# Optimization experiments

Hardware: AMD Instinct MI355X
Metric: run time of the kernel (lower is better)

The kernel has to match this reference:

```python
import jax, jax.numpy as jnp
import numpy as np

B, S, M, D, H = 2, 2048, 512, 1024, 16
HD = D // H      # head dim 64
KVC = D // 16    # MLA kv compression dim 64
QC = D // 32     # MLA q compression dim 32
RD = HD          # retrieval (qk) head dim 64
LOOKBACK = 8     # cross_window
EPS = 1e-6


def rmsnorm(x, w):
    return x * jax.lax.rsqrt(jnp.mean(x * x, axis=-1, keepdims=True) + EPS) * w


def setup_inputs():
    key = jax.random.key(0)
    ks = jax.random.split(key, 20)
    g = lambda i, shape: jax.random.normal(ks[i], shape, jnp.float32) * 0.02
    return {
        "x": jax.random.normal(ks[0], (B, S, D), jnp.float32),
        "memory": jax.random.normal(ks[1], (B, M, D), jnp.float32),
        "seg_ids": jnp.sort(jax.random.randint(ks[2], (B, S), 0, M), axis=-1),
        "norm1_w": jnp.ones((D,), jnp.float32),
        "W_dq": g(3, (D, QC)),
        "W_uq": g(4, (QC, H * RD)),
        "W_dkv": g(5, (D, KVC)),
        "W_uk": g(6, (KVC, H * RD)),
        "W_uv": g(7, (KVC, H * HD)),
        "W_o_self": g(8, (H * HD, D)),
        "norm2_w": jnp.ones((D,), jnp.float32),
        "W_q_c": g(9, (D, D)),
        "W_k_c": g(10, (D, D)),
        "W_v_c": g(11, (D, D)),
        "W_o_c": g(12, (D, D)),
        "norm3_w": jnp.ones((D,), jnp.float32),
        "W_gate": g(13, (D, 4 * D)),
        "W_up": g(14, (D, 4 * D)),
        "W_down": g(15, (4 * D, D)),
    }


def reference(x, memory, seg_ids, norm1_w, W_dq, W_uq, W_dkv, W_uk, W_uv,
              W_o_self, norm2_w, W_q_c, W_k_c, W_v_c, W_o_c, norm3_w,
              W_gate, W_up, W_down):
    # ---- MLA causal self-attention (low-rank compressed q/kv) ----
    h = rmsnorm(x, norm1_w)
    q = ((h @ W_dq) @ W_uq).reshape(B, S, H, RD)
    c_kv = h @ W_dkv                                  # [B,S,KVC]
    k = (c_kv @ W_uk).reshape(B, S, H, RD)
    v = (c_kv @ W_uv).reshape(B, S, H, HD)
    scores = jnp.einsum('bihd,bjhd->bhij', q, k) / np.float32(np.sqrt(RD))
    causal = jnp.tril(jnp.ones((S, S), bool))
    scores = jnp.where(causal, scores, -jnp.inf)
    attn = jax.nn.softmax(scores, axis=-1)
    o = jnp.einsum('bhij,bjhd->bihd', attn, v).reshape(B, S, H * HD)
    x = x + o @ W_o_self
    # ---- segment sliding-window cross-attention ----
    h = rmsnorm(x, norm2_w)
    qc = (h @ W_q_c).reshape(B, S, H, HD)
    kc = (memory @ W_k_c).reshape(B, M, H, HD)
    vc = (memory @ W_v_c).reshape(B, M, H, HD)
    sc = jnp.einsum('bihd,bjhd->bhij', qc, kc) / np.float32(np.sqrt(HD))
    kv_pos = jnp.arange(M)
    seg = seg_ids[:, :, None]                          # [B,S,1]
    allowed = (kv_pos[None, None, :] <= seg) & (kv_pos[None, None, :] >= seg - LOOKBACK)
    sc = jnp.where(allowed[:, None, :, :], sc, -jnp.inf)
    ac = jax.nn.softmax(sc, axis=-1)
    oc = jnp.einsum('bhij,bjhd->bihd', ac, vc).reshape(B, S, D)
    x = x + oc @ W_o_c
    # ---- SwiGLU FFN ----
    h = rmsnorm(x, norm3_w)
    x = x + (jax.nn.silu(h @ W_gate) * (h @ W_up)) @ W_down
    return x
```

## Files before the change

### kernel.cpp

```cpp
#include <hip/hip_runtime.h>
#include <stdint.h>

typedef unsigned short U16;
typedef __bf16 bf16x8 __attribute__((ext_vector_type(8)));
typedef unsigned short us8 __attribute__((ext_vector_type(8)));
typedef float f32x4 __attribute__((ext_vector_type(4)));

__device__ __forceinline__ U16 f2bf(float f) {
    unsigned u = __builtin_bit_cast(unsigned, f);
    unsigned r = (u + 0x7fff + ((u >> 16) & 1)) >> 16;
    return (U16)r;
}
__device__ __forceinline__ U16 f2bf_fast(float f) {
    return (U16)((__builtin_bit_cast(unsigned, f) + 0x8000u) >> 16);
}
__device__ __forceinline__ float bf2f(U16 v) {
    return __builtin_bit_cast(float, (unsigned)v << 16);
}
__device__ __forceinline__ bf16x8 ld8(const U16* p) { return __builtin_bit_cast(bf16x8, *(const us8*)p); }

__device__ __forceinline__ void async16(const U16* g, U16* l) {
    auto* gp = (const __attribute__((address_space(1))) U16*)g;
    auto* lp = (__attribute__((address_space(3))) U16*)(uintptr_t)(uint32_t)(uintptr_t)l;
    __builtin_amdgcn_global_load_lds(gp, lp, 16, 0, 0);
}

struct WEnt { const float* src; U16* dst; int K, N, Kpad, Npad, koff, noff, tiles; };
struct WTable { WEnt e[13]; };

__global__ __launch_bounds__(256) void wtrans_all(WTable t) {
    int bx = blockIdx.x, ei = 0;
    while (bx >= t.e[ei].tiles) { bx -= t.e[ei].tiles; ei++; }
    const WEnt E = t.e[ei];
    const int ntn = E.Npad >> 5;
    const int n0 = (bx % ntn) * 32, k0 = (bx / ntn) * 32;
    __shared__ float tile[32][33];
    const int tx = threadIdx.x & 31, ty = threadIdx.x >> 5;
#pragma unroll
    for (int i = 0; i < 4; i++) {
        int kk = k0 + ty + i * 8, n = n0 + tx;
        int k = kk - E.koff;
        float v = (k >= 0 && k < E.K && n < E.N) ? E.src[(size_t)k * E.N + n] : 0.f;
        tile[ty + i * 8][tx] = v;
    }
    __syncthreads();
#pragma unroll
    for (int i = 0; i < 4; i++) {
        int n = n0 + ty + i * 8, kk = k0 + tx;
        E.dst[(size_t)(E.noff + n) * E.Kpad + kk] = f2bf(tile[tx][ty + i * 8]);
    }
}

__global__ __launch_bounds__(256) void f2bf_k(const float* __restrict__ in, U16* __restrict__ out, int n) {
    int i = (blockIdx.x * 256 + threadIdx.x) * 4;
    if (i < n) {
        float4 v = *(const float4*)(in + i);
        out[i + 0] = f2bf(v.x); out[i + 1] = f2bf(v.y);
        out[i + 2] = f2bf(v.z); out[i + 3] = f2bf(v.w);
    }
}

__global__ __launch_bounds__(256) void cq_reduce(const float* __restrict__ p, U16* __restrict__ out) {
    int i = (blockIdx.x * 256 + threadIdx.x) * 4;
    const float4 a = *(const float4*)(p + i);
    const float4 b = *(const float4*)(p + 524288 + i);
    const float4 c = *(const float4*)(p + 2 * 524288 + i);
    const float4 d = *(const float4*)(p + 3 * 524288 + i);
    out[i + 0] = f2bf(a.x + b.x + c.x + d.x);
    out[i + 1] = f2bf(a.y + b.y + c.y + d.y);
    out[i + 2] = f2bf(a.z + b.z + c.z + d.z);
    out[i + 3] = f2bf(a.w + b.w + c.w + d.w);
}

__global__ __launch_bounds__(256) void rmsnorm_k(const float* __restrict__ x, const float* __restrict__ w,
                                                 U16* __restrict__ h) {
    const int row = blockIdx.x, tid = threadIdx.x;
    const float4 v = *(const float4*)(x + (size_t)row * 1024 + tid * 4);
    float ss = v.x * v.x + v.y * v.y + v.z * v.z + v.w * v.w;
#pragma unroll
    for (int o = 32; o > 0; o >>= 1) ss += __shfl_xor(ss, o);
    __shared__ float red[4];
    if ((tid & 63) == 0) red[tid >> 6] = ss;
    __syncthreads();
    float tot = red[0] + red[1] + red[2] + red[3];
    float sc = rsqrtf(tot * (1.0f / 1024.0f) + 1e-6f);
    const float4 wv = *(const float4*)(w + tid * 4);
    U16* hp = h + (size_t)row * 1024 + tid * 4;
    hp[0] = f2bf(v.x * sc * wv.x); hp[1] = f2bf(v.y * sc * wv.y);
    hp[2] = f2bf(v.z * sc * wv.z); hp[3] = f2bf(v.w * sc * wv.w);
}

__global__ __launch_bounds__(256) void qkuv_gemm(const U16* __restrict__ A, const U16* __restrict__ Wuqk,
                                                 const U16* __restrict__ Wuv,
                                                 U16* __restrict__ qkb, U16* __restrict__ vt) {
    __shared__ __align__(16) U16 As[2][128 * 32];
    __shared__ __align__(16) U16 Bs[2][128 * 32];
    __shared__ __align__(16) U16 Ts[4][64 * 80];
    const int tid = threadIdx.x;
    const bool isuv = blockIdx.x >= 16;
    const U16* Bt = isuv ? Wuv : Wuqk;
    const int n0 = (isuv ? blockIdx.x - 16 : blockIdx.x) * 128;
    const int m0 = blockIdx.y * 128;
    const int wave = tid >> 6, lane = tid & 63, l16 = lane & 15, quad = lane >> 4;
    const int wm = (wave >> 1) * 64, wn = (wave & 1) * 64;
    const int sr = lane >> 2, sc = (lane & 3) * 8;
    const U16* gA = A + (size_t)(m0 + wave * 32 + sr) * 128 + sc;
    const U16* gB = Bt + (size_t)(n0 + wave * 32 + sr) * 128 + sc;
    f32x4 acc[4][4] = {};
    for (int kt = 0; kt < 128; kt += 64) {
        __syncthreads();
#pragma unroll
        for (int p = 0; p < 2; p++) {
            const int o = kt + p * 32;
            async16(gA + o, &As[p][(wave * 32) * 32]);
            async16(gA + 16 * 128 + o, &As[p][(wave * 32 + 16) * 32]);
            async16(gB + o, &Bs[p][(wave * 32) * 32]);
            async16(gB + 16 * 128 + o, &Bs[p][(wave * 32 + 16) * 32]);
        }
        __syncthreads();
#pragma unroll
        for (int p = 0; p < 2; p++) {
            bf16x8 af[4], bfr[4];
#pragma unroll
            for (int i = 0; i < 4; i++) {
                af[i]  = ld8(&As[p][(wm + i * 16 + l16) * 32 + quad * 8]);
                bfr[i] = ld8(&Bs[p][(wn + i * 16 + l16) * 32 + quad * 8]);
            }
#pragma unroll
            for (int mi = 0; mi < 4; mi++)
#pragma unroll
                for (int ni = 0; ni < 4; ni++)
                    acc[mi][ni] = __builtin_amdgcn_mfma_f32_16x16x32_bf16(af[mi], bfr[ni], acc[mi][ni], 0, 0, 0);
        }
    }
    if (isuv) {
        U16* T = Ts[wave];
#pragma unroll
        for (int mi = 0; mi < 4; mi++)
#pragma unroll
            for (int ni = 0; ni < 4; ni++)
#pragma unroll
                for (int r = 0; r < 4; r++)
                    T[(ni * 16 + l16) * 80 + mi * 16 + quad * 4 + r] = f2bf(acc[mi][ni][r]);
#pragma unroll
        for (int c = 0; c < 8; c++) {
            int nloc = (lane >> 3) + 8 * c, mloc = (lane & 7) * 8;
            us8 v = *(const us8*)&T[nloc * 80 + mloc];
            *(us8*)&vt[(size_t)(n0 + wn + nloc) * 4096 + (m0 + wm + mloc)] = v;
        }
    } else {
#pragma unroll
        for (int mi = 0; mi < 4; mi++)
#pragma unroll
            for (int r = 0; r < 4; r++) {
                int m = m0 + wm + mi * 16 + quad * 4 + r;
#pragma unroll
                for (int ni = 0; ni < 4; ni++)
                    qkb[(size_t)m * 2048 + n0 + wn + ni * 16 + l16] = f2bf(acc[mi][ni][r]);
            }
    }
}

template <int EPI>
__global__ __launch_bounds__(256) void gemm_m64(const U16* __restrict__ A, const U16* __restrict__ Bt,
                                                void* __restrict__ Cout, const float* __restrict__ resid,
                                                int M, int N, int K, int lda, int ldb, int ldc) {
    __shared__ __align__(16) U16 As[4][64 * 32];
    __shared__ __align__(16) U16 Bs[4][128 * 32];
    const int tid = threadIdx.x;
    const int m0 = blockIdx.y * 64, n0 = blockIdx.x * 128;
    const int k0 = blockIdx.z * K;
    const int wave = tid >> 6, lane = tid & 63, l16 = lane & 15, quad = lane >> 4;
    const int wm = (wave >> 1) * 32, wn = (wave & 1) * 64;
    const int sr = lane >> 2, sc = (lane & 3) * 8;
    const U16* gA = A + (size_t)(m0 + wave * 16 + sr) * lda + sc + k0;
    const U16* gB = Bt + (size_t)(n0 + wave * 32 + sr) * ldb + sc + k0;
    f32x4 acc[2][4] = {};
    for (int kt = 0; kt < K; kt += 128) {
        __syncthreads();
#pragma unroll
        for (int p = 0; p < 4; p++) {
            const int o = kt + p * 32;
            async16(gA + o, &As[p][(wave * 16) * 32]);
            async16(gB + o, &Bs[p][(wave * 32) * 32]);
            async16(gB + (size_t)16 * ldb + o, &Bs[p][(wave * 32 + 16) * 32]);
        }
        __syncthreads();
#pragma unroll
        for (int p = 0; p < 4; p++) {
            bf16x8 af[2], bfr[4];
#pragma unroll
            for (int i = 0; i < 2; i++)
                af[i] = ld8(&As[p][(wm + i * 16 + l16) * 32 + quad * 8]);
#pragma unroll
            for (int i = 0; i < 4; i++)
                bfr[i] = ld8(&Bs[p][(wn + i * 16 + l16) * 32 + quad * 8]);
#pragma unroll
            for (int mi = 0; mi < 2; mi++)
#pragma unroll
                for (int ni = 0; ni < 4; ni++)
                    acc[mi][ni] = __builtin_amdgcn_mfma_f32_16x16x32_bf16(af[mi], bfr[ni], acc[mi][ni], 0, 0, 0);
        }
    }
#pragma unroll
    for (int mi = 0; mi < 2; mi++) {
#pragma unroll
        for (int r = 0; r < 4; r++) {
            int m = m0 + wm + mi * 16 + quad * 4 + r;
#pragma unroll
            for (int ni = 0; ni < 4; ni++) {
                int n = n0 + wn + ni * 16 + l16;
                float val = acc[mi][ni][r];
                if (EPI == 0) ((U16*)Cout)[(size_t)m * ldc + n] = f2bf(val);
                else if (EPI == 1) ((float*)Cout)[(size_t)m * ldc + n] = resid[(size_t)m * ldc + n] + val;
                else if (EPI == 5) ((float*)Cout)[(size_t)blockIdx.z * 524288 + (size_t)m * ldc + n] = val;
            }
        }
    }
}

__global__ __launch_bounds__(256) void qckv_gemm(const U16* __restrict__ hbuf, const U16* __restrict__ Wqc,
                                                 const U16* __restrict__ memb, const U16* __restrict__ Wkvc,
                                                 U16* __restrict__ qcb, U16* __restrict__ kvcb) {
    __shared__ __align__(16) U16 As[4][64 * 32];
    __shared__ __align__(16) U16 Bs[4][128 * 32];
    const int tid = threadIdx.x, bid = blockIdx.x;
    const U16 *A, *Bt; U16* C; int m0, n0, ldc;
    if (bid < 512) { A = hbuf; Bt = Wqc;  C = qcb;  m0 = (bid >> 3) * 64; n0 = (bid & 7) * 128;  ldc = 1024; }
    else { int b2 = bid - 512; A = memb; Bt = Wkvc; C = kvcb; m0 = (b2 >> 4) * 64; n0 = (b2 & 15) * 128; ldc = 2048; }
    const int wave = tid >> 6, lane = tid & 63, l16 = lane & 15, quad = lane >> 4;
    const int wm = (wave >> 1) * 32, wn = (wave & 1) * 64;
    const int sr = lane >> 2, sc = (lane & 3) * 8;
    const U16* gA = A + (size_t)(m0 + wave * 16 + sr) * 1024 + sc;
    const U16* gB = Bt + (size_t)(n0 + wave * 32 + sr) * 1024 + sc;
    f32x4 acc[2][4] = {};
    for (int kt = 0; kt < 1024; kt += 128) {
        __syncthreads();
#pragma unroll
        for (int p = 0; p < 4; p++) {
            const int o = kt + p * 32;
            async16(gA + o, &As[p][(wave * 16) * 32]);
            async16(gB + o, &Bs[p][(wave * 32) * 32]);
            async16(gB + 16 * 1024 + o, &Bs[p][(wave * 32 + 16) * 32]);
        }
        __syncthreads();
#pragma unroll
        for (int p = 0; p < 4; p++) {
            bf16x8 af[2], bfr[4];
#pragma unroll
            for (int i = 0; i < 2; i++)
                af[i] = ld8(&As[p][(wm + i * 16 + l16) * 32 + quad * 8]);
#pragma unroll
            for (int i = 0; i < 4; i++)
                bfr[i] = ld8(&Bs[p][(wn + i * 16 + l16) * 32 + quad * 8]);
#pragma unroll
            for (int mi = 0; mi < 2; mi++)
#pragma unroll
                for (int ni = 0; ni < 4; ni++)
                    acc[mi][ni] = __builtin_amdgcn_mfma_f32_16x16x32_bf16(af[mi], bfr[ni], acc[mi][ni], 0, 0, 0);
        }
    }
#pragma unroll
    for (int mi = 0; mi < 2; mi++)
#pragma unroll
        for (int r = 0; r < 4; r++) {
            int m = m0 + wm + mi * 16 + quad * 4 + r;
#pragma unroll
            for (int ni = 0; ni < 4; ni++)
                C[(size_t)m * ldc + n0 + wn + ni * 16 + l16] = f2bf(acc[mi][ni][r]);
        }
}

__global__ __launch_bounds__(256) void ffn1_fused(const U16* __restrict__ A, const U16* __restrict__ Wgu,
                                                  U16* __restrict__ Cout) {
    __shared__ __align__(16) U16 As[2][128 * 32];
    __shared__ __align__(16) U16 Gs[2][64 * 32];
    __shared__ __align__(16) U16 Us[2][64 * 32];
    const int tid = threadIdx.x;
    const int m0 = blockIdx.y * 128, n0 = blockIdx.x * 64;
    const int wave = tid >> 6, lane = tid & 63, l16 = lane & 15, quad = lane >> 4;
    const int wm = (wave >> 1) * 64, wn = (wave & 1) * 32;
    const int sr = lane >> 2, sc = (lane & 3) * 8;
    const U16* gA = A + (size_t)(m0 + wave * 32 + sr) * 1024 + sc;
    const U16* gG = Wgu + (size_t)(n0 + wave * 16 + sr) * 1024 + sc;
    const U16* gU = gG + (size_t)4096 * 1024;
    f32x4 ag[4][2] = {}, au[4][2] = {};
    for (int kt = 0; kt < 1024; kt += 64) {
        __syncthreads();
#pragma unroll
        for (int p = 0; p < 2; p++) {
            const int o = kt + p * 32;
            async16(gA + o, &As[p][(wave * 32) * 32]);
            async16(gA + 16 * 1024 + o, &As[p][(wave * 32 + 16) * 32]);
            async16(gG + o, &Gs[p][(wave * 16) * 32]);
            async16(gU + o, &Us[p][(wave * 16) * 32]);
        }
        __syncthreads();
#pragma unroll
        for (int p = 0; p < 2; p++) {
            bf16x8 af[4], bg[2], bu[2];
#pragma unroll
            for (int i = 0; i < 4; i++)
                af[i] = ld8(&As[p][(wm + i * 16 + l16) * 32 + quad * 8]);
#pragma unroll
            for (int i = 0; i < 2; i++) {
                bg[i] = ld8(&Gs[p][(wn + i * 16 + l16) * 32 + quad * 8]);
                bu[i] = ld8(&Us[p][(wn + i * 16 + l16) * 32 + quad * 8]);
            }
#pragma unroll
            for (int mi = 0; mi < 4; mi++)
#pragma unroll
                for (int ni = 0; ni < 2; ni++) {
                    ag[mi][ni] = __builtin_amdgcn_mfma_f32_16x16x32_bf16(af[mi], bg[ni], ag[mi][ni], 0, 0, 0);
                    au[mi][ni] = __builtin_amdgcn_mfma_f32_16x16x32_bf16(af[mi], bu[ni], au[mi][ni], 0, 0, 0);
                }
        }
    }
#pragma unroll
    for (int mi = 0; mi < 4; mi++) {
#pragma unroll
        for (int r = 0; r < 4; r++) {
            int m = m0 + wm + mi * 16 + quad * 4 + r;
#pragma unroll
            for (int ni = 0; ni < 2; ni++) {
                int n = n0 + wn + ni * 16 + l16;
                float g = ag[mi][ni][r], u = au[mi][ni][r];
                float act = g / (1.f + __expf(-g)) * u;
                Cout[(size_t)m * 4096 + n] = f2bf(act);
            }
        }
    }
}

__global__ __launch_bounds__(256) void flash_self3(const U16* __restrict__ QK, const U16* __restrict__ Vt,
                                                   U16* __restrict__ Og) {
    __shared__ __align__(16) U16 Ps[4 * 1280];
    __shared__ float Ored[4 * 2080];
    __shared__ float Lred[128];
    const int wave = threadIdx.x >> 6, lane = threadIdx.x & 63;
    const int l16 = lane & 15, quad = lane >> 4;
    const int bx = blockIdx.x;
    const int t = 63 - (bx >> 5);
    const int bh = bx & 31, b = bh >> 4, h = bh & 15;
    const int q0 = t * 32;
    const size_t rowQ0 = (size_t)(b * 2048 + q0 + l16) * 2048 + h * 64;
    const size_t rowQ1 = rowQ0 + 16 * 2048;
    bf16x8 aq[2][2];
    aq[0][0] = ld8(QK + rowQ0 + quad * 8);  aq[0][1] = ld8(QK + rowQ0 + 32 + quad * 8);
    aq[1][0] = ld8(QK + rowQ1 + quad * 8);  aq[1][1] = ld8(QK + rowQ1 + 32 + quad * 8);
    const U16* Kbase = QK + (size_t)(b * 2048) * 2048 + 1024 + h * 64;
    const U16* Vbase = Vt + (size_t)(h * 64) * 4096 + b * 2048;
    f32x4 o[2][4] = {};
    float ls[2][4] = {};
    U16* Pw = &Ps[wave * 1280];
    const int prd = l16 * 40 + ((quad ^ (l16 >> 2)) << 3);
    const int jend = q0 + 32;
    for (int j0 = wave * 32; j0 < jend; j0 += 128) {
        const U16* kp = Kbase + (size_t)j0 * 2048;
        bf16x8 b00 = ld8(kp + (size_t)l16 * 2048 + quad * 8);
        bf16x8 b01 = ld8(kp + (size_t)l16 * 2048 + 32 + quad * 8);
        bf16x8 b10 = ld8(kp + (size_t)(16 + l16) * 2048 + quad * 8);
        bf16x8 b11 = ld8(kp + (size_t)(16 + l16) * 2048 + 32 + quad * 8);
        bf16x8 v0 = ld8(Vbase + (size_t)(0  + l16) * 4096 + j0 + quad * 8);
        bf16x8 v1 = ld8(Vbase + (size_t)(16 + l16) * 4096 + j0 + quad * 8);
        bf16x8 v2 = ld8(Vbase + (size_t)(32 + l16) * 4096 + j0 + quad * 8);
        bf16x8 v3 = ld8(Vbase + (size_t)(48 + l16) * 4096 + j0 + quad * 8);
        f32x4 s[2][2] = {};
#pragma unroll
        for (int g = 0; g < 2; g++) {
            s[g][0] = __builtin_amdgcn_mfma_f32_16x16x32_bf16(aq[g][0], b00, s[g][0], 0, 0, 0);
            s[g][0] = __builtin_amdgcn_mfma_f32_16x16x32_bf16(aq[g][1], b01, s[g][0], 0, 0, 0);
            s[g][1] = __builtin_amdgcn_mfma_f32_16x16x32_bf16(aq[g][0], b10, s[g][1], 0, 0, 0);
            s[g][1] = __builtin_amdgcn_mfma_f32_16x16x32_bf16(aq[g][1], b11, s[g][1], 0, 0, 0);
        }
        float p0[2][4], p1[2][4];
        if (j0 + 32 >= jend) {
#pragma unroll
            for (int g = 0; g < 2; g++)
#pragma unroll
                for (int r = 0; r < 4; r++) {
                    int qg = q0 + g * 16 + quad * 4 + r;
                    p0[g][r] = (j0 + l16 <= qg) ? __expf(fminf(s[g][0][r] * 0.125f, 30.f)) : 0.f;
                    p1[g][r] = (j0 + 16 + l16 <= qg) ? __expf(fminf(s[g][1][r] * 0.125f, 30.f)) : 0.f;
                }
        } else {
#pragma unroll
            for (int g = 0; g < 2; g++)
#pragma unroll
                for (int r = 0; r < 4; r++) {
                    p0[g][r] = __expf(fminf(s[g][0][r] * 0.125f, 30.f));
                    p1[g][r] = __expf(fminf(s[g][1][r] * 0.125f, 30.f));
                }
        }
#pragma unroll
        for (int g = 0; g < 2; g++)
#pragma unroll
            for (int r = 0; r < 4; r++) {
                ls[g][r] += p0[g][r] + p1[g][r];
                int row = quad * 4 + r;
                Pw[g * 640 + row * 40 + ((((l16 >> 3) + 0) ^ quad) << 3) + (l16 & 7)] = f2bf_fast(p0[g][r]);
                Pw[g * 640 + row * 40 + ((((l16 >> 3) + 2) ^ quad) << 3) + (l16 & 7)] = f2bf_fast(p1[g][r]);
            }
#pragma unroll
        for (int g = 0; g < 2; g++) {
            bf16x8 ap = ld8(&Pw[g * 640 + prd]);
            o[g][0] = __builtin_amdgcn_mfma_f32_16x16x32_bf16(ap, v0, o[g][0], 0, 0, 0);
            o[g][1] = __builtin_amdgcn_mfma_f32_16x16x32_bf16(ap, v1, o[g][1], 0, 0, 0);
            o[g][2] = __builtin_amdgcn_mfma_f32_16x16x32_bf16(ap, v2, o[g][2], 0, 0, 0);
            o[g][3] = __builtin_amdgcn_mfma_f32_16x16x32_bf16(ap, v3, o[g][3], 0, 0, 0);
        }
    }
    float* Or = &Ored[wave * 2080];
#pragma unroll
    for (int g = 0; g < 2; g++) {
#pragma unroll
        for (int dg = 0; dg < 4; dg++)
#pragma unroll
            for (int r = 0; r < 4; r++)
                Or[(g * 16 + quad * 4 + r) * 65 + dg * 16 + l16] = o[g][dg][r];
#pragma unroll
        for (int r = 0; r < 4; r++) {
            float v = ls[g][r];
            v += __shfl_xor(v, 1); v += __shfl_xor(v, 2);
            v += __shfl_xor(v, 4); v += __shfl_xor(v, 8);
            if (l16 == 0) Lred[wave * 32 + g * 16 + quad * 4 + r] = v;
        }
    }
    __syncthreads();
    const int q = threadIdx.x >> 3, d0 = (threadIdx.x & 7) * 8;
    float l = Lred[q] + Lred[32 + q] + Lred[64 + q] + Lred[96 + q];
    float inv = 1.0f / l;
    us8 outv;
#pragma unroll
    for (int i = 0; i < 8; i++) {
        int idx = q * 65 + d0 + i;
        float s = Ored[idx] + Ored[2080 + idx] + Ored[4160 + idx] + Ored[6240 + idx];
        outv[i] = f2bf(s * inv);
    }
    *(us8*)(Og + (size_t)(b * 2048 + q0 + q) * 1024 + h * 64 + d0) = outv;
}

__global__ __launch_bounds__(256) void cross_attn(const U16* __restrict__ qc, const U16* __restrict__ kvc,
                                                  const int* __restrict__ seg_ids, U16* __restrict__ oc) {
    const int tok = blockIdx.x;
    const int b = tok >> 11;
    const int w = threadIdx.x >> 6, lane = threadIdx.x & 63;
    const int h = blockIdx.y * 4 + w;
    const int seg = seg_ids[tok];
    const size_t qoff = (size_t)tok * 1024 + h * 64 + lane;
    float q = bf2f(qc[qoff]);
    float s[9];
#pragma unroll
    for (int jj = 0; jj < 9; jj++) {
        int j = seg - 8 + jj;
        float sc = -INFINITY;
        if (j >= 0) {
            float kv = bf2f(kvc[((size_t)(b * 512) + j) * 2048 + h * 64 + lane]);
            sc = q * kv;
            sc += __shfl_xor(sc, 1); sc += __shfl_xor(sc, 2); sc += __shfl_xor(sc, 4);
            sc += __shfl_xor(sc, 8); sc += __shfl_xor(sc, 16); sc += __shfl_xor(sc, 32);
            sc *= 0.125f;
        }
        s[jj] = sc;
    }
    float m = s[0];
#pragma unroll
    for (int jj = 1; jj < 9; jj++) m = fmaxf(m, s[jj]);
    float l = 0.f, o = 0.f;
#pragma unroll
    for (int jj = 0; jj < 9; jj++) {
        int j = seg - 8 + jj;
        if (j >= 0) {
            float p = __expf(s[jj] - m);
            l += p;
            o += p * bf2f(kvc[((size_t)(b * 512) + j) * 2048 + 1024 + h * 64 + lane]);
        }
    }
    oc[qoff] = f2bf(o / l);
}

extern "C" void kernel_launch(void* const* d_in, const int* in_sizes, int n_in,
                              void* d_out, int out_size, void* d_ws, size_t ws_size,
                              hipStream_t stream) {
    const float* x      = (const float*)d_in[0];
    const float* memory = (const float*)d_in[1];
    const int*   seg    = (const int*)d_in[2];
    const float* n1w    = (const float*)d_in[3];
    const float* W_dq   = (const float*)d_in[4];
    const float* W_uq   = (const float*)d_in[5];
    const float* W_dkv  = (const float*)d_in[6];
    const float* W_uk   = (const float*)d_in[7];
    const float* W_uv   = (const float*)d_in[8];
    const float* W_os   = (const float*)d_in[9];
    const float* n2w    = (const float*)d_in[10];
    const float* W_qc   = (const float*)d_in[11];
    const float* W_kc   = (const float*)d_in[12];
    const float* W_vc   = (const float*)d_in[13];
    const float* W_oc   = (const float*)d_in[14];
    const float* n3w    = (const float*)d_in[15];
    const float* W_gate = (const float*)d_in[16];
    const float* W_up   = (const float*)d_in[17];
    const float* W_down = (const float*)d_in[18];
    (void)in_sizes; (void)n_in; (void)out_size; (void)ws_size;

    char* ws = (char*)d_ws;
    size_t off = 0;
    auto alloc = [&](size_t bytes) -> void* {
        void* p = ws + off;
        off += (bytes + 255) & ~(size_t)255;
        return p;
    };
    const size_t MB = 1024 * 1024;
    U16* hbuf     = (U16*)alloc(8 * MB);
    float* x1     = (float*)alloc(16 * MB);
    float* x2     = (float*)alloc(16 * MB);
    float* cq32   = (float*)alloc(8 * MB);
    U16* Wt_dqkv  = (U16*)alloc(128 * 1024 * 2);
    U16* Wt_uqk   = (U16*)alloc(2048 * 128 * 2);
    U16* Wt_uv    = (U16*)alloc(1024 * 128 * 2);
    U16* Wt_os    = (U16*)alloc(1024 * 1024 * 2);
    U16* Wt_qc    = (U16*)alloc(1024 * 1024 * 2);
    U16* Wt_kvc   = (U16*)alloc((size_t)2048 * 1024 * 2);
    U16* Wt_oc    = (U16*)alloc(1024 * 1024 * 2);
    U16* Wt_gu    = (U16*)alloc((size_t)8192 * 1024 * 2);
    U16* Wt_down  = (U16*)alloc((size_t)1024 * 4096 * 2);
    U16* mem_bf   = (U16*)alloc(1024 * 1024 * 2);
    char* arena   = ws + off;
    U16* cq  = (U16*)(arena);
    U16* qkb = (U16*)(arena + 1 * MB);
    U16* vt  = (U16*)(arena + 17 * MB);
    U16* ob  = (U16*)(arena + 25 * MB);
    U16* qcb  = (U16*)(arena);
    U16* kvcb = (U16*)(arena + 8 * MB);
    U16* ocb  = (U16*)(arena + 12 * MB);
    U16* gact = (U16*)(arena);

    WTable T;
    int i = 0;
    auto ent = [&](const float* s, U16* d, int K, int N, int Kpad, int Npad, int koff, int noff) {
        T.e[i++] = WEnt{s, d, K, N, Kpad, Npad, koff, noff, (Kpad >> 5) * (Npad >> 5)};
    };
    ent(W_dq,   Wt_dqkv, 1024, 32,   1024, 32,   0,  0);
    ent(W_dkv,  Wt_dqkv, 1024, 64,   1024, 96,   0,  32);
    ent(W_uq,   Wt_uqk,  32,   1024, 128,  1024, 0,  0);
    ent(W_uk,   Wt_uqk,  64,   1024, 128,  1024, 32, 1024);
    ent(W_uv,   Wt_uv,   64,   1024, 128,  1024, 32, 0);
    ent(W_os,   Wt_os,   1024, 1024, 1024, 1024, 0,  0);
    ent(W_qc,   Wt_qc,   1024, 1024, 1024, 1024, 0,  0);
    ent(W_kc,   Wt_kvc,  1024, 1024, 1024, 1024, 0,  0);
    ent(W_vc,   Wt_kvc,  1024, 1024, 1024, 1024, 0,  1024);
    ent(W_oc,   Wt_oc,   1024, 1024, 1024, 1024, 0,  0);
    ent(W_gate, Wt_gu,   1024, 4096, 1024, 4096, 0,  0);
    ent(W_up,   Wt_gu,   1024, 4096, 1024, 4096, 0,  4096);
    ent(W_down, Wt_down, 4096, 1024, 4096, 1024, 0,  0);
    int total_tiles = 0;
    for (int j = 0; j < 13; j++) total_tiles += T.e[j].tiles;
    wtrans_all<<<total_tiles, 256, 0, stream>>>(T);
    f2bf_k<<<1024, 256, 0, stream>>>(memory, mem_bf, 1024 * 1024);

    rmsnorm_k<<<4096, 256, 0, stream>>>(x, n1w, hbuf);
    gemm_m64<5><<<dim3(1, 64, 4), 256, 0, stream>>>(hbuf, Wt_dqkv, cq32, nullptr, 4096, 128, 256, 1024, 1024, 128);
    cq_reduce<<<512, 256, 0, stream>>>(cq32, cq);
    qkuv_gemm<<<dim3(24, 32), 256, 0, stream>>>(cq, Wt_uqk, Wt_uv, qkb, vt);
    flash_self3<<<2048, 256, 0, stream>>>(qkb, vt, ob);
    gemm_m64<1><<<dim3(8, 64), 256, 0, stream>>>(ob, Wt_os, x1, x, 4096, 1024, 1024, 1024, 1024, 1024);

    rmsnorm_k<<<4096, 256, 0, stream>>>(x1, n2w, hbuf);
    qckv_gemm<<<768, 256, 0, stream>>>(hbuf, Wt_qc, mem_bf, Wt_kvc, qcb, kvcb);
    cross_attn<<<dim3(4096, 4), 256, 0, stream>>>(qcb, kvcb, seg, ocb);
    gemm_m64<1><<<dim3(8, 64), 256, 0, stream>>>(ocb, Wt_oc, x2, x1, 4096, 1024, 1024, 1024, 1024, 1024);

    rmsnorm_k<<<4096, 256, 0, stream>>>(x2, n3w, hbuf);
    ffn1_fused<<<dim3(64, 32), 256, 0, stream>>>(hbuf, Wt_gu, gact);
    gemm_m64<1><<<dim3(8, 64), 256, 0, stream>>>(gact, Wt_down, (float*)d_out, x2, 4096, 1024, 4096, 4096, 4096, 1024);
}
```

Baseline: 530.5 us.

## Rewrite fused gate/up FFN GEMM with 256x256 tiles, swizzled LDS, double buffering

Replaces the 128x64 gate/up kernel with a 512-thread kernel that computes a 256-row by 128-column-pair tile (gate and up interleaved across waves), using 64-wide K tiles with an XOR-swizzled LDS layout and a two-stage async prefetch pipeline driven by vmcnt waits. The larger tile raises arithmetic intensity and cuts global reloads of the activation and weights, while the swizzle avoids LDS bank conflicts and setprio hints favour MFMA issue. In exchange it uses 128KB of LDS per block and many accumulator registers, which limits occupancy, and the grid drops to 512 blocks.

New measurement: 514.2 us. 1.03x faster.

```diff
diff --git a/kernel.cpp b/kernel.cpp
--- a/kernel.cpp
+++ b/kernel.cpp
@@ -271,65 +271,139 @@
         }
 }
 
-__global__ __launch_bounds__(256) void ffn1_fused(const U16* __restrict__ A, const U16* __restrict__ Wgu,
-                                                  U16* __restrict__ Cout) {
-    __shared__ __align__(16) U16 As[2][128 * 32];
-    __shared__ __align__(16) U16 Gs[2][64 * 32];
-    __shared__ __align__(16) U16 Us[2][64 * 32];
+__global__ __launch_bounds__(512, 2) void ffn1_8ph(const U16* __restrict__ A, const U16* __restrict__ Wgu,
+                                                   U16* __restrict__ Cout) {
+    __shared__ __align__(16) U16 As[2][256 * 64];
+    __shared__ __align__(16) U16 Bs[2][256 * 64];
     const int tid = threadIdx.x;
-    const int m0 = blockIdx.y * 128, n0 = blockIdx.x * 64;
-    const int wave = tid >> 6, lane = tid & 63, l16 = lane & 15, quad = lane >> 4;
-    const int wm = (wave >> 1) * 64, wn = (wave & 1) * 32;
-    const int sr = lane >> 2, sc = (lane & 3) * 8;
-    const U16* gA = A + (size_t)(m0 + wave * 32 + sr) * 1024 + sc;
-    const U16* gG = Wgu + (size_t)(n0 + wave * 16 + sr) * 1024 + sc;
-    const U16* gU = gG + (size_t)4096 * 1024;
-    f32x4 ag[4][2] = {}, au[4][2] = {};
-    for (int kt = 0; kt < 1024; kt += 64) {
-        __syncthreads();
-#pragma unroll
-        for (int p = 0; p < 2; p++) {
-            const int o = kt + p * 32;
-            async16(gA + o, &As[p][(wave * 32) * 32]);
-            async16(gA + 16 * 1024 + o, &As[p][(wave * 32 + 16) * 32]);
-            async16(gG + o, &Gs[p][(wave * 16) * 32]);
-            async16(gU + o, &Us[p][(wave * 16) * 32]);
-        }
-        __syncthreads();
-#pragma unroll
-        for (int p = 0; p < 2; p++) {
-            bf16x8 af[4], bg[2], bu[2];
-#pragma unroll
-            for (int i = 0; i < 4; i++)
-                af[i] = ld8(&As[p][(wm + i * 16 + l16) * 32 + quad * 8]);
-#pragma unroll
-            for (int i = 0; i < 2; i++) {
-                bg[i] = ld8(&Gs[p][(wn + i * 16 + l16) * 32 + quad * 8]);
-                bu[i] = ld8(&Us[p][(wn + i * 16 + l16) * 32 + quad * 8]);
+    const int wid = tid >> 6, lane = tid & 63;
+    const int l16 = lane & 15, quad = lane >> 4;
+    const int n0 = blockIdx.x * 128;
+    const int m0 = blockIdx.y * 256;
+    const int wr = wid >> 2, wc = wid & 3;
+    const int wm = wr * 128;
+    const int wn = wc * 64;
+    const int srow = lane >> 3;
+    const int schunk = (lane & 7) ^ srow;
+    const U16* gA = A + (size_t)(m0 + wid * 32 + srow) * 1024 + schunk * 8;
+    const U16* gB = Wgu + (size_t)((wid & 1) * 4096 + n0 + (wid >> 1) * 32 + srow) * 1024 + schunk * 8;
+
+    auto STAGE = [&](int buf, int kt) {
+        U16* la = &As[buf][(wid * 32) * 64];
+        U16* lb = &Bs[buf][(wid * 32) * 64];
+        const U16* pa = gA + kt;
+        const U16* pb = gB + kt;
+#pragma unroll
+        for (int j = 0; j < 4; ++j) {
+            async16(pa + j * 8 * 1024, la + j * 8 * 64);
+            async16(pb + j * 8 * 1024, lb + j * 8 * 64);
+        }
+    };
+
+    f32x4 acc[8][4] = {};
+
+    auto TILE = [&](int buf) {
+        const U16* Ab = &As[buf][0];
+        const U16* Bb = &Bs[buf][0];
+        const int cx = l16 & 7;
+        bf16x8 a0[4][2], a1[4][2], b0[2][2], b1[2][2];
+#pragma unroll
+        for (int mi = 0; mi < 4; ++mi)
+#pragma unroll
+            for (int kh = 0; kh < 2; ++kh)
+                a0[mi][kh] = ld8(&Ab[(wm + mi * 16 + l16) * 64 + (((kh * 4 + quad) ^ cx) << 3)]);
+#pragma unroll
+        for (int ni = 0; ni < 2; ++ni)
+#pragma unroll
+            for (int kh = 0; kh < 2; ++kh)
+                b0[ni][kh] = ld8(&Bb[(wn + ni * 16 + l16) * 64 + (((kh * 4 + quad) ^ cx) << 3)]);
+#pragma unroll
+        for (int ni = 0; ni < 2; ++ni)
+#pragma unroll
+            for (int kh = 0; kh < 2; ++kh)
+                b1[ni][kh] = ld8(&Bb[(wn + 32 + ni * 16 + l16) * 64 + (((kh * 4 + quad) ^ cx) << 3)]);
+        __builtin_amdgcn_s_setprio(1);
+#pragma unroll
+        for (int mi = 0; mi < 4; ++mi)
+#pragma unroll
+            for (int ni = 0; ni < 2; ++ni)
+#pragma unroll
+                for (int kh = 0; kh < 2; ++kh)
+                    acc[mi][ni] = __builtin_amdgcn_mfma_f32_16x16x32_bf16(a0[mi][kh], b0[ni][kh], acc[mi][ni], 0, 0, 0);
+        __builtin_amdgcn_s_setprio(0);
+#pragma unroll
+        for (int mi = 0; mi < 4; ++mi)
+#pragma unroll
+            for (int kh = 0; kh < 2; ++kh)
+                a1[mi][kh] = ld8(&Ab[(wm + 64 + mi * 16 + l16) * 64 + (((kh * 4 + quad) ^ cx) << 3)]);
+        __builtin_amdgcn_s_setprio(1);
+#pragma unroll
+        for (int mi = 0; mi < 4; ++mi)
+#pragma unroll
+            for (int ni = 0; ni < 2; ++ni)
+#pragma unroll
+                for (int kh = 0; kh < 2; ++kh)
+                    acc[mi][2 + ni] = __builtin_amdgcn_mfma_f32_16x16x32_bf16(a0[mi][kh], b1[ni][kh], acc[mi][2 + ni], 0, 0, 0);
+        __builtin_amdgcn_s_setprio(0);
+        __builtin_amdgcn_s_setprio(1);
+#pragma unroll
+        for (int mi = 0; mi < 4; ++mi)
+#pragma unroll
+            for (int ni = 0; ni < 2; ++ni)
+#pragma unroll
+                for (int kh = 0; kh < 2; ++kh)
+                    acc[4 + mi][2 + ni] = __builtin_amdgcn_mfma_f32_16x16x32_bf16(a1[mi][kh], b1[ni][kh], acc[4 + mi][2 + ni], 0, 0, 0);
+        __builtin_amdgcn_s_setprio(0);
+        __builtin_amdgcn_s_setprio(1);
+#pragma unroll
+        for (int mi = 0; mi < 4; ++mi)
+#pragma unroll
+            for (int ni = 0; ni < 2; ++ni)
+#pragma unroll
+                for (int kh = 0; kh < 2; ++kh)
+                    acc[4 + mi][ni] = __builtin_amdgcn_mfma_f32_16x16x32_bf16(a1[mi][kh], b0[ni][kh], acc[4 + mi][ni], 0, 0, 0);
+        __builtin_amdgcn_s_setprio(0);
+    };
+
+    STAGE(0, 0);
+    STAGE(1, 64);
+#pragma unroll 1
+    for (int t2 = 0; t2 < 7; ++t2) {
+        asm volatile("s_waitcnt vmcnt(8)" ::: "memory");
+        __builtin_amdgcn_s_barrier();
+        __builtin_amdgcn_sched_barrier(0);
+        TILE(0);
+        __builtin_amdgcn_s_barrier();
+        STAGE(0, (2 * t2 + 2) * 64);
+        asm volatile("s_waitcnt vmcnt(8)" ::: "memory");
+        __builtin_amdgcn_s_barrier();
+        __builtin_amdgcn_sched_barrier(0);
+        TILE(1);
+        __builtin_amdgcn_s_barrier();
+        STAGE(1, (2 * t2 + 3) * 64);
+    }
+    asm volatile("s_waitcnt vmcnt(8)" ::: "memory");
+    __builtin_amdgcn_s_barrier();
+    __builtin_amdgcn_sched_barrier(0);
+    TILE(0);
+    asm volatile("s_waitcnt vmcnt(0)" ::: "memory");
+    __builtin_amdgcn_s_barrier();
+    __builtin_amdgcn_sched_barrier(0);
+    TILE(1);
+
+#pragma unroll
+    for (int mi = 0; mi < 8; ++mi)
+#pragma unroll
+        for (int r = 0; r < 4; ++r) {
+            int m = m0 + wm + mi * 16 + quad * 4 + r;
+#pragma unroll
+            for (int ni = 0; ni < 2; ++ni) {
+                int col = n0 + wc * 32 + ni * 16 + l16;
+                float g = acc[mi][ni][r], u = acc[mi][ni + 2][r];
+                float act = g / (1.f + __expf(-g)) * u;
+                Cout[(size_t)m * 4096 + col] = f2bf(act);
             }
-#pragma unroll
-            for (int mi = 0; mi < 4; mi++)
-#pragma unroll
-                for (int ni = 0; ni < 2; ni++) {
-                    ag[mi][ni] = __builtin_amdgcn_mfma_f32_16x16x32_bf16(af[mi], bg[ni], ag[mi][ni], 0, 0, 0);
-                    au[mi][ni] = __builtin_amdgcn_mfma_f32_16x16x32_bf16(af[mi], bu[ni], au[mi][ni], 0, 0, 0);
-                }
-        }
-    }
-#pragma unroll
-    for (int mi = 0; mi < 4; mi++) {
-#pragma unroll
-        for (int r = 0; r < 4; r++) {
-            int m = m0 + wm + mi * 16 + quad * 4 + r;
-#pragma unroll
-            for (int ni = 0; ni < 2; ni++) {
-                int n = n0 + wn + ni * 16 + l16;
-                float g = ag[mi][ni][r], u = au[mi][ni][r];
-                float act = g / (1.f + __expf(-g)) * u;
-                Cout[(size_t)m * 4096 + n] = f2bf(act);
-            }
-        }
-    }
+        }
 }
 
 __global__ __launch_bounds__(256) void flash_self3(const U16* __restrict__ QK, const U16* __restrict__ Vt,
@@ -571,6 +645,6 @@
     gemm_m64<1><<<dim3(8, 64), 256, 0, stream>>>(ocb, Wt_oc, x2, x1, 4096, 1024, 1024, 1024, 1024, 1024);
 
     rmsnorm_k<<<4096, 256, 0, stream>>>(x2, n3w, hbuf);
-    ffn1_fused<<<dim3(64, 32), 256, 0, stream>>>(hbuf, Wt_gu, gact);
+    ffn1_8ph<<<dim3(32, 16), 512, 0, stream>>>(hbuf, Wt_gu, gact);
     gemm_m64<1><<<dim3(8, 64), 256, 0, stream>>>(gact, Wt_down, (float*)d_out, x2, 4096, 1024, 4096, 4096, 4096, 1024);
 }
```
